# Kernel tuning notes

Measured on AMD Instinct MI355X. Metric: run time of the kernel, lower is better.

The kernel has to match this reference:

```python
import jax, jax.numpy as jnp
import numpy as np

B, S, D, H = 2, 2048, 1024, 16
HD = D // H
SCALE = HD ** -0.5


def _xavier(key, fan_out, fan_in):
    limit = (6.0 / (fan_in + fan_out)) ** 0.5
    return jax.random.uniform(key, (fan_out, fan_in), jnp.float32, -limit, limit)


def setup_inputs() -> dict:
    key = jax.random.key(0)
    ks = jax.random.split(key, 11)
    return {
        "q": jax.random.normal(ks[0], (B, S, D), jnp.float32),
        "k": jax.random.normal(ks[1], (B, S, D), jnp.float32),
        "v": jax.random.normal(ks[2], (B, S, D), jnp.float32),
        "Wq": _xavier(ks[3], D, D), "bq": jnp.zeros((D,), jnp.float32),
        "Wk": _xavier(ks[4], D, D), "bk": jnp.zeros((D,), jnp.float32),
        "Wv": _xavier(ks[5], D, D), "bv": jnp.zeros((D,), jnp.float32),
        "Wo": _xavier(ks[6], D, D), "bo": jnp.zeros((D,), jnp.float32),
    }


def reference(q, k, v, Wq, bq, Wk, bk, Wv, bv, Wo, bo):
    # projections: torch Linear is x @ W.T + b
    def split_heads(x):  # [B,S,D] -> [B,H,S,HD]
        return x.reshape(B, S, H, HD).transpose(0, 2, 1, 3)

    qh = split_heads(q @ Wq.T + bq)
    kh = split_heads(k @ Wk.T + bk)
    vh = split_heads(v @ Wv.T + bv)

    scores = jnp.einsum('bhqd,bhkd->bhqk', qh, kh) * SCALE  # [B,H,S,S]
    attn = jax.nn.softmax(scores, axis=-1)
    out = jnp.einsum('bhqk,bhkd->bhqd', attn, vh)  # [B,H,S,HD]
    out = out.transpose(0, 2, 1, 3).reshape(B, S, D)
    return out @ Wo.T + bo
```

## Files before the change

kernel.cpp:

```cpp
#include <hip/hip_runtime.h>
#include <hip/hip_bf16.h>

typedef __attribute__((ext_vector_type(8))) short bf16x8;
typedef __attribute__((ext_vector_type(4))) float f32x4;
typedef __attribute__((ext_vector_type(16))) float f32x16;
typedef unsigned short u16;

#define MFMA16(A,B,C) __builtin_amdgcn_mfma_f32_16x16x32_bf16(A,B,C,0,0,0)
#define MFMA32(A,B,C) __builtin_amdgcn_mfma_f32_32x32x16_bf16(A,B,C,0,0,0)

__device__ __forceinline__ u16 f2bf(float f) {
    union { float f; unsigned u; } x{f};
    unsigned r = x.u + 0x7FFFu + ((x.u >> 16) & 1u);
    return (u16)(r >> 16);
}

__device__ __forceinline__ unsigned cvtpk(float lo, float hi) {
    unsigned r;
    asm("v_cvt_pk_bf16_f32 %0, %1, %2" : "=v"(r) : "v"(lo), "v"(hi));
    return r;
}

__device__ __forceinline__ void gload16(const void* src, void* dst) {
    __builtin_amdgcn_global_load_lds((const __attribute__((address_space(1))) void*)src,
                                     (__attribute__((address_space(3))) void*)dst, 16, 0, 0);
}

__device__ __forceinline__ void xhalf(unsigned lo, unsigned hi2, int hf, unsigned& j0, unsigned& j2) {
#if __has_builtin(__builtin_amdgcn_permlane32_swap)
    auto r = __builtin_amdgcn_permlane32_swap(lo, hi2, false, false);
    j0 = r[0]; j2 = r[1];
#else
    unsigned olo = (unsigned)__shfl_xor((int)lo, 32);
    unsigned ohi = (unsigned)__shfl_xor((int)hi2, 32);
    j0 = hf ? ohi : lo;
    j2 = hf ? hi2 : olo;
#endif
}

__global__ __launch_bounds__(256)
void cvt_all(const float* __restrict__ q, const float* __restrict__ k, const float* __restrict__ v,
             const float* __restrict__ Wq, const float* __restrict__ Wk,
             const float* __restrict__ Wv, const float* __restrict__ Wo,
             u16* __restrict__ oq, u16* __restrict__ ok, u16* __restrict__ ov,
             u16* __restrict__ ow) {
    int blk = blockIdx.x;
    const float* s;
    u16* o;
    if (blk < 6144) {
        int which = blk >> 11, lb = blk & 2047;
        s = (which == 0 ? q : (which == 1 ? k : v)) + (size_t)lb * 2048;
        o = (which == 0 ? oq : (which == 1 ? ok : ov)) + (size_t)lb * 2048;
    } else {
        int wblk = blk - 6144;
        int which = wblk >> 9, lb = wblk & 511;
        s = (which == 0 ? Wq : (which == 1 ? Wk : (which == 2 ? Wv : Wo))) + (size_t)lb * 2048;
        o = ow + (size_t)which * 1048576 + (size_t)lb * 2048;
    }
    size_t base = (size_t)threadIdx.x * 8;
    float4 v0 = *(const float4*)(s + base);
    float4 v1 = *(const float4*)(s + base + 4);
    bf16x8 rv;
    rv[0] = (short)f2bf(v0.x); rv[1] = (short)f2bf(v0.y); rv[2] = (short)f2bf(v0.z); rv[3] = (short)f2bf(v0.w);
    rv[4] = (short)f2bf(v1.x); rv[5] = (short)f2bf(v1.y); rv[6] = (short)f2bf(v1.z); rv[7] = (short)f2bf(v1.w);
    *(bf16x8*)(o + base) = rv;
}

template<int MODE>
__device__ __forceinline__ void gemm_body(u16* gsm, const u16* __restrict__ A, const u16* __restrict__ W,
                                          const float* __restrict__ bias, void* __restrict__ Cout,
                                          float scale) {
    u16* Asl = gsm;
    u16* Wsl = gsm + 16384;
    const int t = threadIdx.x;
    const int lane = t & 63, w = t >> 6;
    const int g = lane >> 4, c = lane & 15;
    const int bm = blockIdx.y * 128, bn = blockIdx.x * 64;
    const int wr = (w >> 1) * 64, wc = (w & 1) * 32;

    f32x4 acc[4][2];
    #pragma unroll
    for (int i = 0; i < 4; ++i) {
        acc[i][0] = f32x4{0.f, 0.f, 0.f, 0.f};
        acc[i][1] = f32x4{0.f, 0.f, 0.f, 0.f};
    }

#define GS(buf, k0)                                                                         \
    {                                                                                       \
        _Pragma("unroll")                                                                   \
        for (int i = 0; i < 4; ++i) {                                                       \
            int off = i * 4096 + w * 1024 + lane * 16;                                      \
            int row = off >> 7, sl = (off >> 4) & 7;                                        \
            gload16(A + (size_t)(bm + row) * 1024 + (k0) + ((sl ^ (row & 7)) << 3),         \
                    Asl + (buf) * 8192 + i * 2048 + w * 512);                               \
        }                                                                                   \
        _Pragma("unroll")                                                                   \
        for (int i = 0; i < 2; ++i) {                                                       \
            int off = i * 4096 + w * 1024 + lane * 16;                                      \
            int row = off >> 7, sl = (off >> 4) & 7;                                        \
            gload16(W + (size_t)(bn + row) * 1024 + (k0) + ((sl ^ (row & 7)) << 3),         \
                    Wsl + (buf) * 4096 + i * 2048 + w * 512);                               \
        }                                                                                   \
    }

    GS(0, 0);
    __syncthreads();
    int cur = 0;

    for (int k0 = 0; k0 < 1024; k0 += 64) {
        if (k0 < 960) GS(cur ^ 1, k0 + 64);
        #pragma unroll
        for (int ks = 0; ks < 2; ++ks) {
            bf16x8 af[4], bfr[2];
            #pragma unroll
            for (int rf = 0; rf < 4; ++rf) {
                int row = wr + rf * 16 + c;
                int col = (ks * 64 + g * 16) ^ ((row & 7) << 4);
                af[rf] = *(const bf16x8*)((const char*)Asl + cur * 16384 + row * 128 + col);
            }
            #pragma unroll
            for (int cf = 0; cf < 2; ++cf) {
                int row = wc + cf * 16 + c;
                int col = (ks * 64 + g * 16) ^ ((row & 7) << 4);
                bfr[cf] = *(const bf16x8*)((const char*)Wsl + cur * 8192 + row * 128 + col);
            }
            __builtin_amdgcn_s_setprio(1);
            #pragma unroll
            for (int rf = 0; rf < 4; ++rf)
                #pragma unroll
                for (int cf = 0; cf < 2; ++cf)
                    acc[rf][cf] = MFMA16(af[rf], bfr[cf], acc[rf][cf]);
            __builtin_amdgcn_s_setprio(0);
        }
        __syncthreads();
        cur ^= 1;
    }
#undef GS

    if (MODE == 2) {
        u16* trp = gsm;
        #pragma unroll
        for (int rf = 0; rf < 4; ++rf)
            #pragma unroll
            for (int cf = 0; cf < 2; ++cf) {
                int d = wc + cf * 16 + c;
                float bv = bias[bn + d];
                unsigned p0 = cvtpk(acc[rf][cf][0] + bv, acc[rf][cf][1] + bv);
                unsigned p1 = cvtpk(acc[rf][cf][2] + bv, acc[rf][cf][3] + bv);
                *(uint2*)&trp[d * 136 + wr + rf * 16 + 4 * g] = make_uint2(p0, p1);
            }
        __syncthreads();
        const int hb = bn >> 6, bb = bm >> 11, sb = bm & 2047;
        u16* vt = (u16*)Cout;
        #pragma unroll
        for (int i = 0; i < 4; ++i) {
            int fl = t + 256 * i;
            int d = fl >> 4, ch = fl & 15;
            bf16x8 vv = *(const bf16x8*)&trp[d * 136 + ch * 8];
            *(bf16x8*)(vt + ((size_t)((bb * 16 + hb) * 64 + d)) * 2048 + sb + ch * 8) = vv;
        }
        return;
    }

    #pragma unroll
    for (int rf = 0; rf < 4; ++rf) {
        #pragma unroll
        for (int cf = 0; cf < 2; ++cf) {
            int nCol = bn + wc + cf * 16 + c;
            float bv = bias[nCol];
            #pragma unroll
            for (int r = 0; r < 4; ++r) {
                int row = bm + wr + rf * 16 + 4 * g + r;
                float val = (acc[rf][cf][r] + bv) * scale;
                if (MODE == 1) ((float*)Cout)[(size_t)row * 1024 + nCol] = val;
                else           ((u16*)Cout)[(size_t)row * 1024 + nCol] = f2bf(val);
            }
        }
    }
}

__global__ __launch_bounds__(256)
void gemm_qkv(const u16* __restrict__ Ab, const u16* __restrict__ Wb,
              const float* __restrict__ b0, const float* __restrict__ b1, const float* __restrict__ b2,
              u16* __restrict__ Qp, u16* __restrict__ Kp, u16* __restrict__ Vtb, float qscale) {
    __shared__ u16 gsm[24576];
    int z = blockIdx.z;
    if (z == 0)      gemm_body<0>(gsm, Ab,           Wb,           b0, Qp,  qscale);
    else if (z == 1) gemm_body<0>(gsm, Ab + 4194304, Wb + 1048576, b1, Kp,  1.f);
    else             gemm_body<2>(gsm, Ab + 8388608, Wb + 2097152, b2, Vtb, 1.f);
}

__global__ __launch_bounds__(256)
void gemm_o(const u16* __restrict__ A, const u16* __restrict__ W,
            const float* __restrict__ bias, float* __restrict__ out) {
    __shared__ u16 gsm[24576];
    gemm_body<1>(gsm, A, W, bias, out, 1.f);
}

__global__ __launch_bounds__(512, 4)
void attn_mfma(const u16* __restrict__ Qp, const u16* __restrict__ Kp,
               const u16* __restrict__ Vt, u16* __restrict__ AO) {
    __shared__ u16 smem[32768];

    const int t = threadIdx.x, lane = t & 63, w = t >> 6;
    const int wl = w & 3, half = w >> 2;
    const int c5 = lane & 31, hf = lane >> 5;

    const int id = blockIdx.x;
    const int xcd = id & 7, slot = id >> 3;
    const int hd = xcd * 4 + (slot >> 4);
    const int b = hd >> 4, h = hd & 15;
    const int qw = (slot & 15) * 128 + wl * 32;

    bf16x8 qfr[4];
    #pragma unroll
    for (int ks = 0; ks < 4; ++ks)
        qfr[ks] = *(const bf16x8*)(Qp + (size_t)(b * 2048 + qw + c5) * 1024 + h * 64 + ks * 16 + hf * 8);

    f32x16 oacc[2], lacc;
    #pragma unroll
    for (int j = 0; j < 16; ++j) { oacc[0][j] = 0.f; oacc[1][j] = 0.f; lacc[j] = 0.f; }

    bf16x8 ones;
    #pragma unroll
    for (int j = 0; j < 8; ++j) ones[j] = (short)0x3F80;

#define STAGE(buf, it)                                                                              \
    {                                                                                               \
        int row = t >> 3, sl = t & 7;                                                               \
        _Pragma("unroll")                                                                           \
        for (int i = 0; i < 2; ++i) {                                                               \
            int kti = i * 16 + (it);                                                                \
            const u16* srck = Kp + (size_t)(b * 2048 + kti * 64 + row) * 1024 + h * 64 +            \
                              ((sl ^ (row & 7)) << 3);                                              \
            gload16(srck, smem + i * 8192 + (buf) * 4096 + w * 512);                                \
            const u16* srcv = Vt + ((size_t)((b * 16 + h) * 64 + row)) * 2048 + kti * 64 +          \
                              ((sl ^ (row & 7)) << 3);                                              \
            gload16(srcv, smem + 16384 + i * 8192 + (buf) * 4096 + w * 512);                        \
        }                                                                                           \
    }

    STAGE(0, 0);
    __syncthreads();
    int cur = 0;

    for (int it = 0; it < 16; ++it) {
        if (it < 15) STAGE(cur ^ 1, it + 1);
        const char* kbase = (const char*)smem + half * 16384 + cur * 8192;
        const char* vbase = (const char*)smem + 32768 + half * 16384 + cur * 8192;

        #pragma unroll
        for (int kf = 0; kf < 2; ++kf) {
            f32x16 s;
            #pragma unroll
            for (int j = 0; j < 16; ++j) s[j] = 0.f;
            const int krow = kf * 32 + c5;
            const int ksw = (krow & 7) << 4;
            __builtin_amdgcn_s_setprio(1);
            #pragma unroll
            for (int ks = 0; ks < 4; ++ks) {
                bf16x8 ka = *(const bf16x8*)(kbase + krow * 128 + ((ks * 32 + hf * 16) ^ ksw));
                s = MFMA32(ka, qfr[ks], s);
            }
            __builtin_amdgcn_s_setprio(0);

            #pragma unroll
            for (int j = 0; j < 16; ++j) s[j] = exp2f(s[j]);
            unsigned wd[8];
            #pragma unroll
            for (int j = 0; j < 8; ++j) wd[j] = cvtpk(s[2 * j], s[2 * j + 1]);

            union { unsigned u[4]; bf16x8 v; } p0, p1;
            xhalf(wd[0], wd[2], hf, p0.u[0], p0.u[2]);
            xhalf(wd[1], wd[3], hf, p0.u[1], p0.u[3]);
            xhalf(wd[4], wd[6], hf, p1.u[0], p1.u[2]);
            xhalf(wd[5], wd[7], hf, p1.u[1], p1.u[3]);

            __builtin_amdgcn_s_setprio(1);
            #pragma unroll
            for (int pp = 0; pp < 2; ++pp) {
                bf16x8 pB = pp ? p1.v : p0.v;
                const int kc = kf * 64 + pp * 32 + hf * 16;
                #pragma unroll
                for (int df = 0; df < 2; ++df) {
                    int vrow = df * 32 + c5;
                    bf16x8 va = *(const bf16x8*)(vbase + vrow * 128 + (kc ^ ((vrow & 7) << 4)));
                    oacc[df] = MFMA32(va, pB, oacc[df]);
                }
                lacc = MFMA32(ones, pB, lacc);
            }
            __builtin_amdgcn_s_setprio(0);
        }

        __syncthreads();
        cur ^= 1;
    }

    float* fs = (float*)smem;
    const int pbase = wl * 2112;
    if (half) {
        #pragma unroll
        for (int df = 0; df < 2; ++df)
            #pragma unroll
            for (int j = 0; j < 16; ++j)
                fs[pbase + (df * 16 + j) * 64 + lane] = oacc[df][j];
        fs[pbase + 2048 + lane] = lacc[0];
    }
    __syncthreads();
    if (!half) {
        #pragma unroll
        for (int df = 0; df < 2; ++df)
            #pragma unroll
            for (int j = 0; j < 16; ++j)
                oacc[df][j] += fs[pbase + (df * 16 + j) * 64 + lane];
        const float inv = 1.f / (lacc[0] + fs[pbase + 2048 + lane]);

        char* pw = (char*)smem + 33792 + wl * 4096;
        #pragma unroll
        for (int df = 0; df < 2; ++df)
            #pragma unroll
            for (int rq = 0; rq < 4; ++rq) {
                unsigned p0 = cvtpk(oacc[df][rq * 4 + 0] * inv, oacc[df][rq * 4 + 1] * inv);
                unsigned p1 = cvtpk(oacc[df][rq * 4 + 2] * inv, oacc[df][rq * 4 + 3] * inv);
                int dbyte = df * 64 + rq * 16 + hf * 8;
                *(uint2*)(pw + c5 * 128 + (dbyte ^ ((c5 & 7) << 4))) = make_uint2(p0, p1);
            }
        #pragma unroll
        for (int i = 0; i < 4; ++i) {
            int fl = lane + 64 * i;
            int q = fl >> 3, ch = fl & 7;
            bf16x8 vv = *(const bf16x8*)(pw + q * 128 + ((ch * 16) ^ ((q & 7) << 4)));
            *(bf16x8*)(AO + (size_t)(b * 2048 + qw + q) * 1024 + h * 64 + ch * 8) = vv;
        }
    }
}

extern "C" void kernel_launch(void* const* d_in, const int* in_sizes, int n_in,
                              void* d_out, int out_size, void* d_ws, size_t ws_size,
                              hipStream_t stream) {
    const float* q  = (const float*)d_in[0];
    const float* k  = (const float*)d_in[1];
    const float* v  = (const float*)d_in[2];
    const float* Wq = (const float*)d_in[3];
    const float* bq = (const float*)d_in[4];
    const float* Wk = (const float*)d_in[5];
    const float* bk = (const float*)d_in[6];
    const float* Wv = (const float*)d_in[7];
    const float* bv = (const float*)d_in[8];
    const float* Wo = (const float*)d_in[9];
    const float* bo = (const float*)d_in[10];

    const size_t NE = 4194304;
    u16* ws = (u16*)d_ws;
    u16* xq = ws;
    u16* xk = ws + NE;
    u16* xv = ws + 2 * NE;
    u16* Wb = ws + 3 * NE;
    u16* Qp = ws + 4 * NE;
    u16* Kp = ws + 5 * NE;
    u16* Vtb = ws + 6 * NE;
    u16* AO = xk;

    const float CS = 0.125f * 1.4426950408889634f;

    cvt_all<<<8192, 256, 0, stream>>>(q, k, v, Wq, Wk, Wv, Wo, xq, xk, xv, Wb);

    gemm_qkv<<<dim3(16, 32, 3), 256, 0, stream>>>(ws, Wb, bq, bk, bv, Qp, Kp, Vtb, CS);

    attn_mfma<<<512, 512, 0, stream>>>(Qp, Kp, Vtb, AO);

    gemm_o<<<dim3(16, 32), 256, 0, stream>>>(AO, Wb + 3145728, bo, (float*)d_out);
}
```

Baseline: 121.6 us.

## Software-pipeline QK^T and PV across iterations with triple-buffered V tiles

Restructures the attention inner loop so the PV matmul for the second key fragment is deferred into the next iteration and interleaved with the next QK^T, letting the exp/convert work overlap with MFMA issue. V tiles move from a double buffer to a triple buffer in LDS so the previous tile stays valid while the next is staged, which raises shared memory from 64KB to 80KB per block. The larger LDS footprint may reduce how many blocks fit per CU against the launch bound of 4, and the deferred P fragments need extra registers.

```diff
diff --git a/kernel.cpp b/kernel.cpp
--- a/kernel.cpp
+++ b/kernel.cpp
@@ -200,7 +200,7 @@
 __global__ __launch_bounds__(512, 4)
 void attn_mfma(const u16* __restrict__ Qp, const u16* __restrict__ Kp,
                const u16* __restrict__ Vt, u16* __restrict__ AO) {
-    __shared__ u16 smem[32768];
+    __shared__ u16 smem[40960];
 
     const int t = threadIdx.x, lane = t & 63, w = t >> 6;
     const int wl = w & 3, half = w >> 2;
@@ -225,7 +225,7 @@
     #pragma unroll
     for (int j = 0; j < 8; ++j) ones[j] = (short)0x3F80;
 
-#define STAGE(buf, it)                                                                              \
+#define STAGE(kbuf, vbuf, it)                                                                       \
     {                                                                                               \
         int row = t >> 3, sl = t & 7;                                                               \
         _Pragma("unroll")                                                                           \
@@ -233,69 +233,98 @@
             int kti = i * 16 + (it);                                                                \
             const u16* srck = Kp + (size_t)(b * 2048 + kti * 64 + row) * 1024 + h * 64 +            \
                               ((sl ^ (row & 7)) << 3);                                              \
-            gload16(srck, smem + i * 8192 + (buf) * 4096 + w * 512);                                \
+            gload16(srck, smem + i * 8192 + (kbuf) * 4096 + w * 512);                               \
             const u16* srcv = Vt + ((size_t)((b * 16 + h) * 64 + row)) * 2048 + kti * 64 +          \
                               ((sl ^ (row & 7)) << 3);                                              \
-            gload16(srcv, smem + 16384 + i * 8192 + (buf) * 4096 + w * 512);                        \
+            gload16(srcv, smem + 16384 + i * 12288 + (vbuf) * 4096 + w * 512);                      \
         }                                                                                           \
     }
 
-    STAGE(0, 0);
+#define QKT(kbase, kf, s)                                                                           \
+    {                                                                                               \
+        _Pragma("unroll")                                                                           \
+        for (int j = 0; j < 16; ++j) (s)[j] = 0.f;                                                  \
+        const int krow = (kf) * 32 + c5;                                                            \
+        const int ksw = (krow & 7) << 4;                                                            \
+        _Pragma("unroll")                                                                           \
+        for (int ks = 0; ks < 4; ++ks) {                                                            \
+            bf16x8 ka = *(const bf16x8*)((kbase) + krow * 128 + ((ks * 32 + hf * 16) ^ ksw));       \
+            (s) = MFMA32(ka, qfr[ks], (s));                                                         \
+        }                                                                                           \
+    }
+
+#define SM(s, pv0, pv1)                                                                             \
+    {                                                                                               \
+        _Pragma("unroll")                                                                           \
+        for (int j = 0; j < 16; ++j) (s)[j] = exp2f((s)[j]);                                        \
+        unsigned wd[8];                                                                             \
+        _Pragma("unroll")                                                                           \
+        for (int j = 0; j < 8; ++j) wd[j] = cvtpk((s)[2 * j], (s)[2 * j + 1]);                      \
+        union { unsigned u[4]; bf16x8 v; } a0, a1;                                                  \
+        xhalf(wd[0], wd[2], hf, a0.u[0], a0.u[2]);                                                  \
+        xhalf(wd[1], wd[3], hf, a0.u[1], a0.u[3]);                                                  \
+        xhalf(wd[4], wd[6], hf, a1.u[0], a1.u[2]);                                                  \
+        xhalf(wd[5], wd[7], hf, a1.u[1], a1.u[3]);                                                  \
+        (pv0) = a0.v; (pv1) = a1.v;                                                                 \
+    }
+
+#define PVOP(vbase, kf, pv0, pv1)                                                                   \
+    {                                                                                               \
+        _Pragma("unroll")                                                                           \
+        for (int pp = 0; pp < 2; ++pp) {                                                            \
+            bf16x8 pB = pp ? (pv1) : (pv0);                                                         \
+            const int kc = (kf) * 64 + pp * 32 + hf * 16;                                           \
+            _Pragma("unroll")                                                                       \
+            for (int df = 0; df < 2; ++df) {                                                        \
+                int vrow = df * 32 + c5;                                                            \
+                bf16x8 va = *(const bf16x8*)((vbase) + vrow * 128 + (kc ^ ((vrow & 7) << 4)));      \
+                oacc[df] = MFMA32(va, pB, oacc[df]);                                                \
+            }                                                                                       \
+            lacc = MFMA32(ones, pB, lacc);                                                          \
+        }                                                                                           \
+    }
+
+    STAGE(0, 0, 0);
     __syncthreads();
-    int cur = 0;
+
+    const char* smb = (const char*)smem;
+    const char* vreg = smb + 32768 + half * 24576;
+    int cur2 = 0, cur3 = 0, nxt3 = 1, prv3 = 2;
+    bf16x8 pc0, pc1;
 
     for (int it = 0; it < 16; ++it) {
-        if (it < 15) STAGE(cur ^ 1, it + 1);
-        const char* kbase = (const char*)smem + half * 16384 + cur * 8192;
-        const char* vbase = (const char*)smem + 32768 + half * 16384 + cur * 8192;
-
-        #pragma unroll
-        for (int kf = 0; kf < 2; ++kf) {
-            f32x16 s;
-            #pragma unroll
-            for (int j = 0; j < 16; ++j) s[j] = 0.f;
-            const int krow = kf * 32 + c5;
-            const int ksw = (krow & 7) << 4;
-            __builtin_amdgcn_s_setprio(1);
-            #pragma unroll
-            for (int ks = 0; ks < 4; ++ks) {
-                bf16x8 ka = *(const bf16x8*)(kbase + krow * 128 + ((ks * 32 + hf * 16) ^ ksw));
-                s = MFMA32(ka, qfr[ks], s);
-            }
-            __builtin_amdgcn_s_setprio(0);
-
-            #pragma unroll
-            for (int j = 0; j < 16; ++j) s[j] = exp2f(s[j]);
-            unsigned wd[8];
-            #pragma unroll
-            for (int j = 0; j < 8; ++j) wd[j] = cvtpk(s[2 * j], s[2 * j + 1]);
-
-            union { unsigned u[4]; bf16x8 v; } p0, p1;
-            xhalf(wd[0], wd[2], hf, p0.u[0], p0.u[2]);
-            xhalf(wd[1], wd[3], hf, p0.u[1], p0.u[3]);
-            xhalf(wd[4], wd[6], hf, p1.u[0], p1.u[2]);
-            xhalf(wd[5], wd[7], hf, p1.u[1], p1.u[3]);
-
-            __builtin_amdgcn_s_setprio(1);
-            #pragma unroll
-            for (int pp = 0; pp < 2; ++pp) {
-                bf16x8 pB = pp ? p1.v : p0.v;
-                const int kc = kf * 64 + pp * 32 + hf * 16;
-                #pragma unroll
-                for (int df = 0; df < 2; ++df) {
-                    int vrow = df * 32 + c5;
-                    bf16x8 va = *(const bf16x8*)(vbase + vrow * 128 + (kc ^ ((vrow & 7) << 4)));
-                    oacc[df] = MFMA32(va, pB, oacc[df]);
-                }
-                lacc = MFMA32(ones, pB, lacc);
-            }
-            __builtin_amdgcn_s_setprio(0);
-        }
+        if (it < 15) STAGE(cur2 ^ 1, nxt3, it + 1);
+        const char* kbase = smb + half * 16384 + cur2 * 8192;
+        const char* vcur = vreg + cur3 * 8192;
+        const char* vprev = vreg + prv3 * 8192;
+
+        f32x16 s0;
+        __builtin_amdgcn_s_setprio(1);
+        QKT(kbase, 0, s0);
+        if (it) PVOP(vprev, 1, pc0, pc1);
+        __builtin_amdgcn_s_setprio(0);
+
+        bf16x8 b00, b01;
+        SM(s0, b00, b01);
+
+        f32x16 s1;
+        __builtin_amdgcn_s_setprio(1);
+        QKT(kbase, 1, s1);
+        PVOP(vcur, 0, b00, b01);
+        __builtin_amdgcn_s_setprio(0);
+
+        SM(s1, pc0, pc1);
 
         __syncthreads();
-        cur ^= 1;
-    }
-
+        prv3 = cur3; cur3 = nxt3; nxt3 = (nxt3 == 2) ? 0 : nxt3 + 1;
+        cur2 ^= 1;
+    }
+    {
+        const char* vprev = vreg + prv3 * 8192;
+        PVOP(vprev, 1, pc0, pc1);
+    }
+
+    __syncthreads();
     float* fs = (float*)smem;
     const int pbase = wl * 2112;
     if (half) {
```

After: 120.9 us. About the same (-0.6%).
